# Kernel optimization log

Measured on AMD Instinct MI355X. Metric: run time of the kernel, lower is better.

## Reference

```python
import jax, jax.numpy as jnp
import numpy as np

N = 50000   # nodes
E = 800000  # edges (before self-loops)
IN = 256    # in_dim
H = 4       # heads
C = 64      # out_dim per head
NEG_SLOPE = 0.2
BN_EPS = 1e-5


def setup_inputs() -> dict:
    key = jax.random.key(0)
    ks = jax.random.split(key, 6)
    feature = jax.random.normal(ks[0], (N, IN), jnp.float32)
    edge_index = jax.random.randint(ks[1], (2, E), 0, N, dtype=jnp.int64)
    W = jax.random.normal(ks[2], (IN, H * C), jnp.float32) * 0.05
    att_src = jax.random.normal(ks[3], (H, C), jnp.float32) * 0.1
    att_dst = jax.random.normal(ks[4], (H, C), jnp.float32) * 0.1
    bias = jnp.zeros((H * C,), jnp.float32)
    gamma = jnp.ones((H * C,), jnp.float32)
    beta = jnp.zeros((H * C,), jnp.float32)
    return {"feature": feature, "edge_index": edge_index, "W": W,
            "att_src": att_src, "att_dst": att_dst, "bias": bias,
            "gamma": gamma, "beta": beta}


def reference(feature, edge_index, W, att_src, att_dst, bias, gamma, beta):
    n = feature.shape[0]
    # linear projection -> [N, H, C]
    x = (feature @ W).reshape(n, H, C)
    # per-node attention logits [N, H]
    a_src = jnp.einsum('nhc,hc->nh', x, att_src)
    a_dst = jnp.einsum('nhc,hc->nh', x, att_dst)
    # add self loops (PyG GATConv default)
    loop = jnp.arange(n, dtype=edge_index.dtype)
    src = jnp.concatenate([edge_index[0], loop])
    dst = jnp.concatenate([edge_index[1], loop])
    # edge attention scores [E+N, H]
    e = jax.nn.leaky_relu(a_src[src] + a_dst[dst], NEG_SLOPE)
    # segment softmax over incoming edges of each dst node
    m = jax.ops.segment_max(e, dst, num_segments=n)
    ex = jnp.exp(e - m[dst])
    denom = jax.ops.segment_sum(ex, dst, num_segments=n)
    alpha = ex / denom[dst]                       # [E+N, H]
    # weighted message aggregation -> [N, H, C]
    msg = x[src] * alpha[:, :, None]
    out = jax.ops.segment_sum(msg, dst, num_segments=n)
    h = out.reshape(n, H * C) + bias
    # batchnorm over nodes (training-mode batch statistics)
    mu = jnp.mean(h, axis=0)
    var = jnp.var(h, axis=0)
    h = (h - mu) * jax.lax.rsqrt(var + BN_EPS) * gamma + beta
    # ELU activation
    h = jax.nn.elu(h)
    # residual (in_dim == out_dim * num_heads)
    return feature + h
```

## Files before the change

kernel.cpp:

```cpp
#include <hip/hip_runtime.h>

#define N_NODES 50000
#define N_EDGES 800000
#define NEG_SLOPE 0.2f
#define BN_EPS  1e-5f

#define CHUNKS 256
#define EDGES_PER_CHUNK 3125
#define NCOARSE 1024
#define NBUCKET 782

typedef short bf16x8 __attribute__((ext_vector_type(8)));
typedef float floatx4 __attribute__((ext_vector_type(4)));

__device__ inline ushort f2bf(float f) {
    union { float f; unsigned u; } v; v.f = f;
    unsigned r = v.u + 0x7fff + ((v.u >> 16) & 1);
    return (ushort)(r >> 16);
}
__device__ inline float bf2f(ushort h) {
    union { unsigned u; float f; } v; v.u = ((unsigned)h) << 16;
    return v.f;
}

__global__ __launch_bounds__(256) void count_wt_kernel(const int* __restrict__ ei,
                                                       const float* __restrict__ W,
                                                       int* __restrict__ counts,
                                                       ushort* __restrict__ Wtb)
{
    __shared__ int hist[NCOARSE];
    const int t = threadIdx.x;
    const int b = blockIdx.x;
    if (b < CHUNKS) {
        for (int j = t; j < NCOARSE; j += 256) hist[j] = 0;
        __syncthreads();
        const int e0 = b * EDGES_PER_CHUNK;
        for (int e = e0 + t; e < e0 + EDGES_PER_CHUNK; e += 256)
            atomicAdd(&hist[ei[N_EDGES + e] >> 6], 1);
        __syncthreads();
        for (int j = t; j < NCOARSE; j += 256)
            counts[j * CHUNKS + b] = hist[j];
    } else {
        const int n = b - CHUNKS;
        Wtb[n * 256 + t] = f2bf(W[t * 256 + n]);
    }
}

__global__ __launch_bounds__(256) void sscan1_kernel(int* __restrict__ counts,
                                                     int* __restrict__ blocksum)
{
    __shared__ int sm[256];
    const int t = threadIdx.x;
    const int i = blockIdx.x * 256 + t;
    const int v = counts[i];
    sm[t] = v;
    __syncthreads();
#pragma unroll
    for (int off = 1; off < 256; off <<= 1) {
        const int u = (t >= off) ? sm[t - off] : 0;
        __syncthreads();
        sm[t] += u;
        __syncthreads();
    }
    counts[i] = sm[t] - v;
    if (t == 255) blocksum[blockIdx.x] = sm[255];
}

__global__ __launch_bounds__(256) void sscan2_kernel(const int* __restrict__ blocksum,
                                                     int* __restrict__ blockbase,
                                                     float* __restrict__ gsum,
                                                     float* __restrict__ gsumsq)
{
    __shared__ int sm[256];
    const int t = threadIdx.x;
    int v[4], loc[4], tot = 0;
#pragma unroll
    for (int j = 0; j < 4; ++j) {
        v[j] = blocksum[t * 4 + j];
        loc[j] = tot;
        tot += v[j];
    }
    sm[t] = tot;
    __syncthreads();
#pragma unroll
    for (int off = 1; off < 256; off <<= 1) {
        const int u = (t >= off) ? sm[t - off] : 0;
        __syncthreads();
        sm[t] += u;
        __syncthreads();
    }
    const int base = sm[t] - tot;
#pragma unroll
    for (int j = 0; j < 4; ++j) blockbase[t * 4 + j] = base + loc[j];
    gsum[t] = 0.f;
    gsumsq[t] = 0.f;
}

__global__ __launch_bounds__(256) void bucket_scatter_kernel(const int* __restrict__ ei,
                                                             const int* __restrict__ counts,
                                                             const int* __restrict__ blockbase,
                                                             uint* __restrict__ tmp)
{
    __shared__ int cursor[NCOARSE];
    const int t = threadIdx.x;
    const int blk = blockIdx.x;
    for (int u = t; u < NCOARSE; u += 256)
        cursor[u] = counts[u * CHUNKS + blk] + blockbase[u];
    __syncthreads();
    const int e0 = blk * EDGES_PER_CHUNK;
    for (int e = e0 + t; e < e0 + EDGES_PER_CHUNK; e += 256) {
        const int src = ei[e];
        const int dst = ei[N_EDGES + e];
        const int pos = atomicAdd(&cursor[dst >> 6], 1);
        tmp[pos] = ((uint)src << 6) | (uint)(dst & 63);
    }
}

__global__ __launch_bounds__(256) void bucket_build_kernel(const uint* __restrict__ tmp,
                                                           const int* __restrict__ blockbase,
                                                           int* __restrict__ offsets,
                                                           int* __restrict__ csr_src)
{
    __shared__ int hist[64];
    __shared__ int sbuf[64];
    __shared__ int cursor[64];
    const int t = threadIdx.x;
    const int b = blockIdx.x;
    const int start = blockbase[b];
    const int end   = blockbase[b + 1];
    if (t < 64) hist[t] = 0;
    __syncthreads();
    for (int e = start + t; e < end; e += 256)
        atomicAdd(&hist[tmp[e] & 63], 1);
    __syncthreads();
    const int v = (t < 64) ? hist[t] : 0;
    if (t < 64) sbuf[t] = v;
    __syncthreads();
#pragma unroll
    for (int off = 1; off < 64; off <<= 1) {
        int u = 0;
        if (t < 64 && t >= off) u = sbuf[t - off];
        __syncthreads();
        if (t < 64) sbuf[t] += u;
        __syncthreads();
    }
    if (t < 64) {
        const int excl = start + sbuf[t] - v;
        cursor[t] = excl;
        const int node = b * 64 + t;
        if (node < N_NODES) offsets[node] = excl;
    }
    if (b == 0 && t == 0) offsets[N_NODES] = N_EDGES;
    __syncthreads();
    for (int e = start + t; e < end; e += 256) {
        const uint p = tmp[e];
        const int pos = atomicAdd(&cursor[p & 63], 1);
        csr_src[pos] = (int)(p >> 6);
    }
}

#define LDSTRIDE 40
__global__ __launch_bounds__(256) void gemm_kernel(const float* __restrict__ A,
                                                   const ushort* __restrict__ Bt,
                                                   const float* __restrict__ att_src,
                                                   const float* __restrict__ att_dst,
                                                   ushort* __restrict__ Xb,
                                                   float* __restrict__ s,
                                                   float* __restrict__ d)
{
    __shared__ ushort As[128 * LDSTRIDE];
    __shared__ ushort Bs[128 * LDSTRIDE];
    const int tid = threadIdx.x;
    const int lane = tid & 63;
    const int wid = tid >> 6;
    const int wm = wid & 1, wn = wid >> 1;
    const int row0 = blockIdx.y * 128;
    const int col0 = blockIdx.x * 128;

    floatx4 acc[4][4] = {};

    const int lr = tid >> 2;
    const int lk = (tid & 3) * 8;

    for (int k0 = 0; k0 < 256; k0 += 32) {
#pragma unroll
        for (int r = 0; r < 2; ++r) {
            const int row = lr + r * 64;
            const int grow = row0 + row;
            union { ushort u[8]; ulonglong2 v; } cv;
            if (grow < N_NODES) {
                const float4 f0 = *(const float4*)(A + (size_t)grow * 256 + k0 + lk);
                const float4 f1 = *(const float4*)(A + (size_t)grow * 256 + k0 + lk + 4);
                cv.u[0] = f2bf(f0.x); cv.u[1] = f2bf(f0.y);
                cv.u[2] = f2bf(f0.z); cv.u[3] = f2bf(f0.w);
                cv.u[4] = f2bf(f1.x); cv.u[5] = f2bf(f1.y);
                cv.u[6] = f2bf(f1.z); cv.u[7] = f2bf(f1.w);
            } else {
                cv.v = ulonglong2{0ull, 0ull};
            }
            *(ulonglong2*)(As + row * LDSTRIDE + lk) = cv.v;
            const ulonglong2 bv = *(const ulonglong2*)(Bt + (size_t)(col0 + row) * 256 + k0 + lk);
            *(ulonglong2*)(Bs + row * LDSTRIDE + lk) = bv;
        }
        __syncthreads();
        const int quad = lane >> 4;
        const int l16 = lane & 15;
        bf16x8 afrag[4], bfrag[4];
#pragma unroll
        for (int mi = 0; mi < 4; ++mi)
            afrag[mi] = *(const bf16x8*)(As + (wm * 64 + mi * 16 + l16) * LDSTRIDE + quad * 8);
#pragma unroll
        for (int ni = 0; ni < 4; ++ni)
            bfrag[ni] = *(const bf16x8*)(Bs + (wn * 64 + ni * 16 + l16) * LDSTRIDE + quad * 8);
#pragma unroll
        for (int mi = 0; mi < 4; ++mi)
#pragma unroll
            for (int ni = 0; ni < 4; ++ni)
                acc[mi][ni] = __builtin_amdgcn_mfma_f32_16x16x32_bf16(afrag[mi], bfrag[ni], acc[mi][ni], 0, 0, 0);
        __syncthreads();
    }

    const int quad = lane >> 4;
    const int l16 = lane & 15;
    const int head = (col0 + wn * 64) >> 6;
    float as_l[4], ad_l[4];
#pragma unroll
    for (int ni = 0; ni < 4; ++ni) {
        const int ch = head * 64 + ni * 16 + l16;
        as_l[ni] = att_src[ch];
        ad_l[ni] = att_dst[ch];
    }
#pragma unroll
    for (int mi = 0; mi < 4; ++mi) {
#pragma unroll
        for (int r = 0; r < 4; ++r) {
            const int grow = row0 + wm * 64 + mi * 16 + quad * 4 + r;
            const bool ok = grow < N_NODES;
            float vs = 0.f, vd = 0.f;
            ushort4 o;
#pragma unroll
            for (int ni = 0; ni < 4; ++ni) {
                const float v = acc[mi][ni][r];
                vs += v * as_l[ni];
                vd += v * ad_l[ni];
                ((ushort*)&o)[ni] = f2bf(v);
            }
            if (ok)
                *(ushort4*)(Xb + (size_t)grow * 256 + head * 64 + l16 * 4) = o;
#pragma unroll
            for (int m = 8; m >= 1; m >>= 1) {
                vs += __shfl_xor(vs, m);
                vd += __shfl_xor(vd, m);
            }
            if (l16 == 0 && ok) {
                s[grow * 4 + head] = vs;
                d[grow * 4 + head] = vd;
            }
        }
    }
}

__global__ __launch_bounds__(256) void aggregate_kernel(const ushort* __restrict__ xb,
                                                        const float* __restrict__ s,
                                                        const float* __restrict__ d,
                                                        const int* __restrict__ offsets,
                                                        const int* __restrict__ csr_src,
                                                        ushort* __restrict__ hagg)
{
    const int wid = threadIdx.x >> 6;
    const int lane = threadIdx.x & 63;
    const int n = blockIdx.x * 4 + wid;
    if (n >= N_NODES) return;
    const int h = lane >> 4;
    const float dn = d[n * 4 + h];
    const float sn = s[n * 4 + h];
    const ushort4 xr = *(const ushort4*)(xb + (size_t)n * 256 + lane * 4);
    float eself = sn + dn;
    eself = eself >= 0.f ? eself : NEG_SLOPE * eself;
    const float pself = __expf(eself);
    float den = pself;
    float a0 = pself * bf2f(xr.x), a1 = pself * bf2f(xr.y);
    float a2 = pself * bf2f(xr.z), a3 = pself * bf2f(xr.w);
    const int e0 = offsets[n];
    const int e1 = offsets[n + 1];
    int e = e0;
    for (; e + 8 <= e1; e += 8) {
        int si[8];
        float lg[8];
        ushort4 xv[8];
#pragma unroll
        for (int j = 0; j < 8; ++j) si[j] = csr_src[e + j];
#pragma unroll
        for (int j = 0; j < 8; ++j) lg[j] = s[si[j] * 4 + h] + dn;
#pragma unroll
        for (int j = 0; j < 8; ++j)
            xv[j] = *(const ushort4*)(xb + (size_t)si[j] * 256 + lane * 4);
#pragma unroll
        for (int j = 0; j < 8; ++j) {
            float l = lg[j];
            l = l >= 0.f ? l : NEG_SLOPE * l;
            const float p = __expf(l);
            den += p;
            a0 += p * bf2f(xv[j].x);
            a1 += p * bf2f(xv[j].y);
            a2 += p * bf2f(xv[j].z);
            a3 += p * bf2f(xv[j].w);
        }
    }
    for (; e < e1; ++e) {
        const int src = csr_src[e];
        float ee = s[src * 4 + h] + dn;
        ee = ee >= 0.f ? ee : NEG_SLOPE * ee;
        const float pe = __expf(ee);
        const ushort4 xs = *(const ushort4*)(xb + (size_t)src * 256 + lane * 4);
        a0 += pe * bf2f(xs.x); a1 += pe * bf2f(xs.y);
        a2 += pe * bf2f(xs.z); a3 += pe * bf2f(xs.w);
        den += pe;
    }
    const float inv = 1.0f / den;
    ushort4 o;
    o.x = f2bf(a0 * inv); o.y = f2bf(a1 * inv);
    o.z = f2bf(a2 * inv); o.w = f2bf(a3 * inv);
    *(ushort4*)(hagg + (size_t)n * 256 + lane * 4) = o;
}

#define BN_BLOCKS 784
__global__ __launch_bounds__(256) void bn_stats_kernel(const ushort* __restrict__ hagg,
                                                       float* __restrict__ gsum,
                                                       float* __restrict__ gsumsq)
{
    const int c = threadIdx.x;
    const int r0 = blockIdx.x * 64;
    float sum = 0.f, sq = 0.f;
#pragma unroll 4
    for (int i = 0; i < 64; ++i) {
        const int r = r0 + i;
        if (r < N_NODES) {
            const float v = bf2f(hagg[(size_t)r * 256 + c]);
            sum += v;
            sq += v * v;
        }
    }
    atomicAdd(&gsum[c], sum);
    atomicAdd(&gsumsq[c], sq);
}

__global__ __launch_bounds__(256) void finalize_kernel(const float* __restrict__ feature,
                                                       const ushort* __restrict__ hagg,
                                                       const float* __restrict__ gsum,
                                                       const float* __restrict__ gsumsq,
                                                       const float* __restrict__ gamma,
                                                       const float* __restrict__ beta,
                                                       float* __restrict__ out)
{
    const int wid = threadIdx.x >> 6;
    const int lane = threadIdx.x & 63;
    const int wgid = blockIdx.x * 4 + wid;
    const int hblk = lane >> 4;
    const int l16 = lane & 15;

    float meanv[4], scalev[4], betav[4];
    int tc[4];
#pragma unroll
    for (int j = 0; j < 4; ++j) {
        const int p = lane * 4 + j;
        tc[j] = hblk * 64 + j * 16 + l16;
        const float m = gsum[p] * (1.0f / N_NODES);
        const float var = gsumsq[p] * (1.0f / N_NODES) - m * m;
        meanv[j] = m;
        scalev[j] = gamma[tc[j]] * rsqrtf(var + BN_EPS);
        betav[j] = beta[tc[j]];
    }
#pragma unroll
    for (int rr = 0; rr < 4; ++rr) {
        const int n = wgid * 4 + rr;
        const ushort4 hv = *(const ushort4*)(hagg + (size_t)n * 256 + lane * 4);
        const float hvf[4] = {bf2f(hv.x), bf2f(hv.y), bf2f(hv.z), bf2f(hv.w)};
#pragma unroll
        for (int j = 0; j < 4; ++j) {
            float r = (hvf[j] - meanv[j]) * scalev[j] + betav[j];
            r = r > 0.f ? r : expm1f(r);
            out[(size_t)n * 256 + tc[j]] = r + feature[(size_t)n * 256 + tc[j]];
        }
    }
}

extern "C" void kernel_launch(void* const* d_in, const int* in_sizes, int n_in,
                              void* d_out, int out_size, void* d_ws, size_t ws_size,
                              hipStream_t stream)
{
    const float* feature = (const float*)d_in[0];
    const int*   ei      = (const int*)d_in[1];
    const float* W       = (const float*)d_in[2];
    const float* att_src = (const float*)d_in[3];
    const float* att_dst = (const float*)d_in[4];
    const float* gamma   = (const float*)d_in[6];
    const float* beta    = (const float*)d_in[7];
    float* out = (float*)d_out;

    char* w = (char*)d_ws;
    auto carve = [&](size_t bytes) {
        char* p = w;
        w += (bytes + 255) & ~(size_t)255;
        return p;
    };
    ushort* Wtb      = (ushort*)carve((size_t)256 * 256 * 2);
    ushort* xb       = (ushort*)carve((size_t)N_NODES * 256 * 2);
    ushort* hagg     = (ushort*)carve((size_t)N_NODES * 256 * 2);
    float*  s        = (float*)carve((size_t)N_NODES * 4 * 4);
    float*  dv       = (float*)carve((size_t)N_NODES * 4 * 4);
    int*    counts   = (int*)carve((size_t)NCOARSE * CHUNKS * 4);
    int*    offsets  = (int*)carve((size_t)(N_NODES + 1) * 4);
    int*    csr_src  = (int*)carve((size_t)N_EDGES * 4);
    int*    blocksum = (int*)carve((size_t)NCOARSE * 4);
    int*    blockbase= (int*)carve((size_t)NCOARSE * 4);
    float*  gsum     = (float*)carve(256 * 4);
    float*  gsumsq   = (float*)carve(256 * 4);
    uint*   tmp      = (uint*)hagg;

    count_wt_kernel<<<512, 256, 0, stream>>>(ei, W, counts, Wtb);
    sscan1_kernel<<<NCOARSE, 256, 0, stream>>>(counts, blocksum);
    sscan2_kernel<<<1, 256, 0, stream>>>(blocksum, blockbase, gsum, gsumsq);
    bucket_scatter_kernel<<<CHUNKS, 256, 0, stream>>>(ei, counts, blockbase, tmp);
    bucket_build_kernel<<<NBUCKET, 256, 0, stream>>>(tmp, blockbase, offsets, csr_src);
    gemm_kernel<<<dim3(2, 391), 256, 0, stream>>>(feature, Wtb, att_src, att_dst, xb, s, dv);
    aggregate_kernel<<<12500, 256, 0, stream>>>(xb, s, dv, offsets, csr_src, hagg);
    bn_stats_kernel<<<BN_BLOCKS, 256, 0, stream>>>(hagg, gsum, gsumsq);
    finalize_kernel<<<3125, 256, 0, stream>>>(feature, hagg, gsum, gsumsq, gamma, beta, out);
}
```

Baseline: 288.6 us.

## Merge CSR build into one cooperative kernel and fuse BN stats into aggregation

The five CSR-construction kernels (count, two scans, bucket scatter, bucket build) become a single cooperative kernel of 1024 blocks separated by grid.sync. This removes several launch boundaries. The batchnorm statistics kernel is removed: aggregation reduces each block's four node rows in shared memory and atomically adds them into 16 striped partial-sum rows, which finalize then reduces. This saves a full re-read of the aggregated features but adds shared-memory traffic and atomics to the aggregation kernel, and it relies on all 1024 blocks being co-resident for the cooperative launch.

Result: slower. 732.1 us (+153.7%).

```diff
diff --git a/kernel.cpp b/kernel.cpp
--- a/kernel.cpp
+++ b/kernel.cpp
@@ -1,4 +1,6 @@
 #include <hip/hip_runtime.h>
+#include <hip/hip_cooperative_groups.h>
+namespace cg = cooperative_groups;
 
 #define N_NODES 50000
 #define N_EDGES 800000
@@ -9,6 +11,7 @@
 #define EDGES_PER_CHUNK 3125
 #define NCOARSE 1024
 #define NBUCKET 782
+#define BNR 16
 
 typedef short bf16x8 __attribute__((ext_vector_type(8)));
 typedef float floatx4 __attribute__((ext_vector_type(4)));
@@ -23,140 +26,131 @@
     return v.f;
 }
 
-__global__ __launch_bounds__(256) void count_wt_kernel(const int* __restrict__ ei,
+__global__ __launch_bounds__(256) void csr_coop_kernel(const int* __restrict__ ei,
                                                        const float* __restrict__ W,
+                                                       ushort* __restrict__ Wtb,
                                                        int* __restrict__ counts,
-                                                       ushort* __restrict__ Wtb)
+                                                       int* __restrict__ blocksum,
+                                                       int* __restrict__ blockbase,
+                                                       uint* __restrict__ tmp,
+                                                       int* __restrict__ offsets,
+                                                       int* __restrict__ csr_src,
+                                                       float* __restrict__ gsum2d,
+                                                       float* __restrict__ gsq2d)
 {
-    __shared__ int hist[NCOARSE];
+    cg::grid_group grid = cg::this_grid();
+    __shared__ int sh[NCOARSE];
+    __shared__ int sh2[64];
+    __shared__ int sh3[64];
     const int t = threadIdx.x;
     const int b = blockIdx.x;
+
     if (b < CHUNKS) {
-        for (int j = t; j < NCOARSE; j += 256) hist[j] = 0;
+        for (int j = t; j < NCOARSE; j += 256) sh[j] = 0;
         __syncthreads();
         const int e0 = b * EDGES_PER_CHUNK;
         for (int e = e0 + t; e < e0 + EDGES_PER_CHUNK; e += 256)
-            atomicAdd(&hist[ei[N_EDGES + e] >> 6], 1);
+            atomicAdd(&sh[ei[N_EDGES + e] >> 6], 1);
         __syncthreads();
         for (int j = t; j < NCOARSE; j += 256)
-            counts[j * CHUNKS + b] = hist[j];
-    } else {
+            counts[j * CHUNKS + b] = sh[j];
+    } else if (b < 2 * CHUNKS) {
         const int n = b - CHUNKS;
         Wtb[n * 256 + t] = f2bf(W[t * 256 + n]);
-    }
-}
-
-__global__ __launch_bounds__(256) void sscan1_kernel(int* __restrict__ counts,
-                                                     int* __restrict__ blocksum)
-{
-    __shared__ int sm[256];
-    const int t = threadIdx.x;
-    const int i = blockIdx.x * 256 + t;
-    const int v = counts[i];
-    sm[t] = v;
-    __syncthreads();
-#pragma unroll
-    for (int off = 1; off < 256; off <<= 1) {
-        const int u = (t >= off) ? sm[t - off] : 0;
-        __syncthreads();
-        sm[t] += u;
-        __syncthreads();
-    }
-    counts[i] = sm[t] - v;
-    if (t == 255) blocksum[blockIdx.x] = sm[255];
-}
-
-__global__ __launch_bounds__(256) void sscan2_kernel(const int* __restrict__ blocksum,
-                                                     int* __restrict__ blockbase,
-                                                     float* __restrict__ gsum,
-                                                     float* __restrict__ gsumsq)
-{
-    __shared__ int sm[256];
-    const int t = threadIdx.x;
-    int v[4], loc[4], tot = 0;
-#pragma unroll
-    for (int j = 0; j < 4; ++j) {
-        v[j] = blocksum[t * 4 + j];
-        loc[j] = tot;
-        tot += v[j];
-    }
-    sm[t] = tot;
-    __syncthreads();
-#pragma unroll
-    for (int off = 1; off < 256; off <<= 1) {
-        const int u = (t >= off) ? sm[t - off] : 0;
-        __syncthreads();
-        sm[t] += u;
-        __syncthreads();
-    }
-    const int base = sm[t] - tot;
-#pragma unroll
-    for (int j = 0; j < 4; ++j) blockbase[t * 4 + j] = base + loc[j];
-    gsum[t] = 0.f;
-    gsumsq[t] = 0.f;
-}
-
-__global__ __launch_bounds__(256) void bucket_scatter_kernel(const int* __restrict__ ei,
-                                                             const int* __restrict__ counts,
-                                                             const int* __restrict__ blockbase,
-                                                             uint* __restrict__ tmp)
-{
-    __shared__ int cursor[NCOARSE];
-    const int t = threadIdx.x;
-    const int blk = blockIdx.x;
-    for (int u = t; u < NCOARSE; u += 256)
-        cursor[u] = counts[u * CHUNKS + blk] + blockbase[u];
-    __syncthreads();
-    const int e0 = blk * EDGES_PER_CHUNK;
-    for (int e = e0 + t; e < e0 + EDGES_PER_CHUNK; e += 256) {
-        const int src = ei[e];
-        const int dst = ei[N_EDGES + e];
-        const int pos = atomicAdd(&cursor[dst >> 6], 1);
-        tmp[pos] = ((uint)src << 6) | (uint)(dst & 63);
-    }
-}
-
-__global__ __launch_bounds__(256) void bucket_build_kernel(const uint* __restrict__ tmp,
-                                                           const int* __restrict__ blockbase,
-                                                           int* __restrict__ offsets,
-                                                           int* __restrict__ csr_src)
-{
-    __shared__ int hist[64];
-    __shared__ int sbuf[64];
-    __shared__ int cursor[64];
-    const int t = threadIdx.x;
-    const int b = blockIdx.x;
-    const int start = blockbase[b];
-    const int end   = blockbase[b + 1];
-    if (t < 64) hist[t] = 0;
-    __syncthreads();
-    for (int e = start + t; e < end; e += 256)
-        atomicAdd(&hist[tmp[e] & 63], 1);
-    __syncthreads();
-    const int v = (t < 64) ? hist[t] : 0;
-    if (t < 64) sbuf[t] = v;
-    __syncthreads();
-#pragma unroll
-    for (int off = 1; off < 64; off <<= 1) {
-        int u = 0;
-        if (t < 64 && t >= off) u = sbuf[t - off];
-        __syncthreads();
-        if (t < 64) sbuf[t] += u;
-        __syncthreads();
-    }
-    if (t < 64) {
-        const int excl = start + sbuf[t] - v;
-        cursor[t] = excl;
-        const int node = b * 64 + t;
-        if (node < N_NODES) offsets[node] = excl;
+    } else if (b < 2 * CHUNKS + 2 * BNR) {
+        const int i = (b - 2 * CHUNKS) * 256 + t;
+        if (i < BNR * 256) gsum2d[i] = 0.f;
+        else               gsq2d[i - BNR * 256] = 0.f;
+    }
+    grid.sync();
+
+    {
+        const int i = b * CHUNKS + t;
+        const int v = counts[i];
+        sh[t] = v;
+        __syncthreads();
+#pragma unroll
+        for (int off = 1; off < 256; off <<= 1) {
+            const int u = (t >= off) ? sh[t - off] : 0;
+            __syncthreads();
+            sh[t] += u;
+            __syncthreads();
+        }
+        counts[i] = sh[t] - v;
+        if (t == 255) blocksum[b] = sh[255];
+    }
+    grid.sync();
+
+    if (b == 0) {
+        int v4[4], loc[4], tot = 0;
+#pragma unroll
+        for (int j = 0; j < 4; ++j) {
+            v4[j] = blocksum[t * 4 + j];
+            loc[j] = tot;
+            tot += v4[j];
+        }
+        sh[t] = tot;
+        __syncthreads();
+#pragma unroll
+        for (int off = 1; off < 256; off <<= 1) {
+            const int u = (t >= off) ? sh[t - off] : 0;
+            __syncthreads();
+            sh[t] += u;
+            __syncthreads();
+        }
+        const int base = sh[t] - tot;
+#pragma unroll
+        for (int j = 0; j < 4; ++j) blockbase[t * 4 + j] = base + loc[j];
+    }
+    grid.sync();
+
+    if (b < CHUNKS) {
+        for (int u = t; u < NCOARSE; u += 256)
+            sh[u] = counts[u * CHUNKS + b] + blockbase[u];
+        __syncthreads();
+        const int e0 = b * EDGES_PER_CHUNK;
+        for (int e = e0 + t; e < e0 + EDGES_PER_CHUNK; e += 256) {
+            const int src = ei[e];
+            const int dst = ei[N_EDGES + e];
+            const int pos = atomicAdd(&sh[dst >> 6], 1);
+            tmp[pos] = ((uint)src << 6) | (uint)(dst & 63);
+        }
+    }
+    grid.sync();
+
+    if (b < NBUCKET) {
+        const int start = blockbase[b];
+        const int end   = blockbase[b + 1];
+        if (t < 64) sh[t] = 0;
+        __syncthreads();
+        for (int e = start + t; e < end; e += 256)
+            atomicAdd(&sh[tmp[e] & 63], 1);
+        __syncthreads();
+        const int v = (t < 64) ? sh[t] : 0;
+        if (t < 64) sh2[t] = v;
+        __syncthreads();
+#pragma unroll
+        for (int off = 1; off < 64; off <<= 1) {
+            int u = 0;
+            if (t < 64 && t >= off) u = sh2[t - off];
+            __syncthreads();
+            if (t < 64) sh2[t] += u;
+            __syncthreads();
+        }
+        if (t < 64) {
+            const int excl = start + sh2[t] - v;
+            sh3[t] = excl;
+            const int node = b * 64 + t;
+            if (node < N_NODES) offsets[node] = excl;
+        }
+        __syncthreads();
+        for (int e = start + t; e < end; e += 256) {
+            const uint p = tmp[e];
+            const int pos = atomicAdd(&sh3[p & 63], 1);
+            csr_src[pos] = (int)(p >> 6);
+        }
     }
     if (b == 0 && t == 0) offsets[N_NODES] = N_EDGES;
-    __syncthreads();
-    for (int e = start + t; e < end; e += 256) {
-        const uint p = tmp[e];
-        const int pos = atomicAdd(&cursor[p & 63], 1);
-        csr_src[pos] = (int)(p >> 6);
-    }
 }
 
 #define LDSTRIDE 40
@@ -265,12 +259,15 @@
                                                         const float* __restrict__ d,
                                                         const int* __restrict__ offsets,
                                                         const int* __restrict__ csr_src,
-                                                        ushort* __restrict__ hagg)
+                                                        ushort* __restrict__ hagg,
+                                                        float* __restrict__ gsum2d,
+                                                        float* __restrict__ gsq2d)
 {
+    __shared__ float s1[4][256];
+    __shared__ float s2[4][256];
     const int wid = threadIdx.x >> 6;
     const int lane = threadIdx.x & 63;
     const int n = blockIdx.x * 4 + wid;
-    if (n >= N_NODES) return;
     const int h = lane >> 4;
     const float dn = d[n * 4 + h];
     const float sn = s[n * 4 + h];
@@ -322,37 +319,42 @@
     o.x = f2bf(a0 * inv); o.y = f2bf(a1 * inv);
     o.z = f2bf(a2 * inv); o.w = f2bf(a3 * inv);
     *(ushort4*)(hagg + (size_t)n * 256 + lane * 4) = o;
-}
-
-#define BN_BLOCKS 784
-__global__ __launch_bounds__(256) void bn_stats_kernel(const ushort* __restrict__ hagg,
-                                                       float* __restrict__ gsum,
-                                                       float* __restrict__ gsumsq)
-{
-    const int c = threadIdx.x;
-    const int r0 = blockIdx.x * 64;
-    float sum = 0.f, sq = 0.f;
-#pragma unroll 4
-    for (int i = 0; i < 64; ++i) {
-        const int r = r0 + i;
-        if (r < N_NODES) {
-            const float v = bf2f(hagg[(size_t)r * 256 + c]);
-            sum += v;
-            sq += v * v;
-        }
-    }
-    atomicAdd(&gsum[c], sum);
-    atomicAdd(&gsumsq[c], sq);
+    const float v0 = bf2f(o.x), v1 = bf2f(o.y), v2 = bf2f(o.z), v3 = bf2f(o.w);
+    s1[wid][lane * 4 + 0] = v0;      s2[wid][lane * 4 + 0] = v0 * v0;
+    s1[wid][lane * 4 + 1] = v1;      s2[wid][lane * 4 + 1] = v1 * v1;
+    s1[wid][lane * 4 + 2] = v2;      s2[wid][lane * 4 + 2] = v2 * v2;
+    s1[wid][lane * 4 + 3] = v3;      s2[wid][lane * 4 + 3] = v3 * v3;
+    __syncthreads();
+    const int t = threadIdx.x;
+    const float ps = s1[0][t] + s1[1][t] + s1[2][t] + s1[3][t];
+    const float pq = s2[0][t] + s2[1][t] + s2[2][t] + s2[3][t];
+    const int row = blockIdx.x & (BNR - 1);
+    atomicAdd(&gsum2d[row * 256 + t], ps);
+    atomicAdd(&gsq2d[row * 256 + t], pq);
 }
 
 __global__ __launch_bounds__(256) void finalize_kernel(const float* __restrict__ feature,
                                                        const ushort* __restrict__ hagg,
-                                                       const float* __restrict__ gsum,
-                                                       const float* __restrict__ gsumsq,
+                                                       const float* __restrict__ gsum2d,
+                                                       const float* __restrict__ gsq2d,
                                                        const float* __restrict__ gamma,
                                                        const float* __restrict__ beta,
                                                        float* __restrict__ out)
 {
+    __shared__ float meanL[256], rstdL[256];
+    const int t = threadIdx.x;
+    float ms = 0.f, qs = 0.f;
+#pragma unroll
+    for (int r = 0; r < BNR; ++r) {
+        ms += gsum2d[r * 256 + t];
+        qs += gsq2d[r * 256 + t];
+    }
+    const float mean = ms * (1.0f / N_NODES);
+    const float var = qs * (1.0f / N_NODES) - mean * mean;
+    meanL[t] = mean;
+    rstdL[t] = rsqrtf(var + BN_EPS);
+    __syncthreads();
+
     const int wid = threadIdx.x >> 6;
     const int lane = threadIdx.x & 63;
     const int wgid = blockIdx.x * 4 + wid;
@@ -365,10 +367,8 @@
     for (int j = 0; j < 4; ++j) {
         const int p = lane * 4 + j;
         tc[j] = hblk * 64 + j * 16 + l16;
-        const float m = gsum[p] * (1.0f / N_NODES);
-        const float var = gsumsq[p] * (1.0f / N_NODES) - m * m;
-        meanv[j] = m;
-        scalev[j] = gamma[tc[j]] * rsqrtf(var + BN_EPS);
+        meanv[j] = meanL[p];
+        scalev[j] = gamma[tc[j]] * rstdL[p];
         betav[j] = beta[tc[j]];
     }
 #pragma unroll
@@ -414,17 +414,18 @@
     int*    csr_src  = (int*)carve((size_t)N_EDGES * 4);
     int*    blocksum = (int*)carve((size_t)NCOARSE * 4);
     int*    blockbase= (int*)carve((size_t)NCOARSE * 4);
-    float*  gsum     = (float*)carve(256 * 4);
-    float*  gsumsq   = (float*)carve(256 * 4);
+    float*  gsum2d   = (float*)carve((size_t)BNR * 256 * 4);
+    float*  gsq2d    = (float*)carve((size_t)BNR * 256 * 4);
     uint*   tmp      = (uint*)hagg;
 
-    count_wt_kernel<<<512, 256, 0, stream>>>(ei, W, counts, Wtb);
-    sscan1_kernel<<<NCOARSE, 256, 0, stream>>>(counts, blocksum);
-    sscan2_kernel<<<1, 256, 0, stream>>>(blocksum, blockbase, gsum, gsumsq);
-    bucket_scatter_kernel<<<CHUNKS, 256, 0, stream>>>(ei, counts, blockbase, tmp);
-    bucket_build_kernel<<<NBUCKET, 256, 0, stream>>>(tmp, blockbase, offsets, csr_src);
+    void* cargs[] = {(void*)&ei, (void*)&W, (void*)&Wtb, (void*)&counts,
+                     (void*)&blocksum, (void*)&blockbase, (void*)&tmp,
+                     (void*)&offsets, (void*)&csr_src,
+                     (void*)&gsum2d, (void*)&gsq2d};
+    hipLaunchCooperativeKernel((void*)csr_coop_kernel, dim3(NCOARSE), dim3(256),
+                               cargs, 0, stream);
     gemm_kernel<<<dim3(2, 391), 256, 0, stream>>>(feature, Wtb, att_src, att_dst, xb, s, dv);
-    aggregate_kernel<<<12500, 256, 0, stream>>>(xb, s, dv, offsets, csr_src, hagg);
-    bn_stats_kernel<<<BN_BLOCKS, 256, 0, stream>>>(hagg, gsum, gsumsq);
-    finalize_kernel<<<3125, 256, 0, stream>>>(feature, hagg, gsum, gsumsq, gamma, beta, out);
-}
+    aggregate_kernel<<<12500, 256, 0, stream>>>(xb, s, dv, offsets, csr_src, hagg,
+                                                gsum2d, gsq2d);
+    finalize_kernel<<<3125, 256, 0, stream>>>(feature, hagg, gsum2d, gsq2d, gamma, beta, out);
+}
```
